# Kernel optimization log

Measured on AMD Instinct MI355X. Metric: run time of the kernel, lower is better.

Reference implementation:

```python
import jax, jax.numpy as jnp
import numpy as np

N_NODES = 50000
N_EDGES = 800000
IN_F = 128
OUT_F = 64
ORDER = 3


def _spmm(edge_index, edge_attr, x):
    # out[row] += edge_attr[e] * x[col]  (COO sparse @ dense)
    row, col = edge_index[0], edge_index[1]
    msgs = x[col] * edge_attr[:, None]          # [E, F] gather + scale
    return jax.ops.segment_sum(msgs, row, num_segments=N_NODES)  # scatter-add


def setup_inputs() -> dict:
    key = jax.random.key(0)
    k1, k2, k3, k4 = jax.random.split(key, 4)
    x = jax.random.normal(k1, (N_NODES, IN_F), dtype=jnp.float32)
    edge_index = jax.random.randint(k2, (2, N_EDGES), 0, N_NODES, dtype=jnp.int64)
    edge_attr = jax.random.uniform(k3, (N_EDGES,), dtype=jnp.float32)
    W = jax.random.normal(k4, (OUT_F, IN_F), dtype=jnp.float32) * (1.0 / np.sqrt(IN_F))
    b = jnp.zeros((OUT_F,), dtype=jnp.float32)
    return {"x": x, "edge_index": edge_index, "edge_attr": edge_attr, "W": W, "b": b}


def reference(x, edge_index, edge_attr, W, b):
    # output = Linear(x); then `order` rounds of spmm aggregation
    out = jnp.einsum("ni,oi->no", x, W) + b      # [N, OUT_F]
    for _ in range(ORDER):
        out = _spmm(edge_index, edge_attr, out)
    return out
```

## Files before the change

kernel.cpp:

```cpp
#include <hip/hip_runtime.h>

#define IN_F   128
#define OUT_F  64
#define GR     64
#define EPB    4096
#define HB     512

typedef float  f32x4  __attribute__((ext_vector_type(4)));
typedef unsigned int u32x2 __attribute__((ext_vector_type(2)));

__device__ __forceinline__ unsigned short f2bf(float f) {
    unsigned int u = __float_as_uint(f);
    u += 0x7fffu + ((u >> 16) & 1u);
    return (unsigned short)(u >> 16);
}
__device__ __forceinline__ float bf2f(unsigned short h) {
    return __uint_as_float(((unsigned int)h) << 16);
}

template <bool BF16OUT>
__global__ __launch_bounds__(256) void gemm_hist_kernel(
    const float* __restrict__ x, const float* __restrict__ W,
    const float* __restrict__ b, void* __restrict__ outv, int N,
    const int* __restrict__ rowi, int* __restrict__ bcnt, int E,
    int gemm_blocks, int hist_blocks) {

    if ((int)blockIdx.x >= gemm_blocks) {
        __shared__ int hcnt[256];
        int t = threadIdx.x;
        hcnt[t] = 0;
        __syncthreads();
        int hb = blockIdx.x - gemm_blocks;
        for (int e = hb * 256 + t; e < E; e += hist_blocks * 256)
            atomicAdd(&hcnt[rowi[e] >> 8], 1);
        __syncthreads();
        if (hcnt[t] > 0) atomicAdd(&bcnt[t], hcnt[t]);
        return;
    }

    __shared__ float xs[GR][IN_F + 4];
    __shared__ float Wt[IN_F][OUT_F + 4];

    const int t = threadIdx.x;
    const int row0 = blockIdx.x * GR;

    for (int i = t; i < OUT_F * (IN_F / 4); i += 256) {
        int o = i & 63;
        int c = i >> 6;
        float4 v = ((const float4*)W)[o * (IN_F / 4) + c];
        Wt[4 * c + 0][o] = v.x;
        Wt[4 * c + 1][o] = v.y;
        Wt[4 * c + 2][o] = v.z;
        Wt[4 * c + 3][o] = v.w;
    }
    for (int i = t; i < GR * (IN_F / 4); i += 256) {
        int r = i >> 5, c = i & 31;
        int gr = row0 + r;
        float4 v = make_float4(0.f, 0.f, 0.f, 0.f);
        if (gr < N) v = ((const float4*)x)[(size_t)gr * (IN_F / 4) + c];
        *(float4*)&xs[r][4 * c] = v;
    }
    __syncthreads();

    const int f0 = (t & 15) * 4;
    const int r0 = (t >> 4) * 4;
    float acc[4][4] = {};

    #pragma unroll 2
    for (int k = 0; k < IN_F; k += 4) {
        float4 xv[4], wv[4];
        #pragma unroll
        for (int i = 0; i < 4; ++i) xv[i] = *(const float4*)&xs[r0 + i][k];
        #pragma unroll
        for (int j = 0; j < 4; ++j) wv[j] = *(const float4*)&Wt[k + j][f0];
        #pragma unroll
        for (int i = 0; i < 4; ++i) {
            #pragma unroll
            for (int j = 0; j < 4; ++j) {
                float wx = j == 0 ? wv[0].x : (j == 1 ? wv[0].y : (j == 2 ? wv[0].z : wv[0].w));
                float wy = j == 0 ? wv[1].x : (j == 1 ? wv[1].y : (j == 2 ? wv[1].z : wv[1].w));
                float wz = j == 0 ? wv[2].x : (j == 1 ? wv[2].y : (j == 2 ? wv[2].z : wv[2].w));
                float ww = j == 0 ? wv[3].x : (j == 1 ? wv[3].y : (j == 2 ? wv[3].z : wv[3].w));
                acc[i][j] = fmaf(xv[i].x, wx, acc[i][j]);
                acc[i][j] = fmaf(xv[i].y, wy, acc[i][j]);
                acc[i][j] = fmaf(xv[i].z, wz, acc[i][j]);
                acc[i][j] = fmaf(xv[i].w, ww, acc[i][j]);
            }
        }
    }

    float4 bv = *(const float4*)&b[f0];
    #pragma unroll
    for (int i = 0; i < 4; ++i) {
        int gr = row0 + r0 + i;
        if (gr < N) {
            float o0 = acc[i][0] + bv.x, o1 = acc[i][1] + bv.y;
            float o2 = acc[i][2] + bv.z, o3 = acc[i][3] + bv.w;
            if (BF16OUT) {
                ushort4 u = { f2bf(o0), f2bf(o1), f2bf(o2), f2bf(o3) };
                *(ushort4*)((unsigned short*)outv + (size_t)gr * OUT_F + f0) = u;
            } else {
                float4 o4 = make_float4(o0, o1, o2, o3);
                *(float4*)((float*)outv + (size_t)gr * OUT_F + f0) = o4;
            }
        }
    }
}

__global__ __launch_bounds__(256) void bscan_kernel(const int* __restrict__ bcnt,
                                                    int* __restrict__ bbase,
                                                    int* __restrict__ bcursor,
                                                    int* __restrict__ rowptr,
                                                    int nb, int N, int E) {
    int t = threadIdx.x;
    int v = (t < nb) ? bcnt[t] : 0;
    int lane = t & 63, w = t >> 6;
    int sum = v;
    #pragma unroll
    for (int off = 1; off < 64; off <<= 1) {
        int x = __shfl_up(sum, off, 64);
        if (lane >= off) sum += x;
    }
    __shared__ int wsum[4];
    if (lane == 63) wsum[w] = sum;
    __syncthreads();
    int woff = 0;
    for (int i = 0; i < w; ++i) woff += wsum[i];
    int excl = sum + woff - v;
    if (t <= nb) bbase[t] = excl;
    if (t < nb)  bcursor[t] = excl;
    if (t == 0)  rowptr[N] = E;
}

__global__ __launch_bounds__(512) void bin_kernel(
    const int* __restrict__ rowi, const int* __restrict__ coli,
    const float* __restrict__ attr, int* __restrict__ bcursor,
    unsigned long long* __restrict__ tmp, int E) {
    __shared__ int cnt[256];
    __shared__ int cur[256];
    __shared__ int gbase[256];
    int t = threadIdx.x;
    int e0 = blockIdx.x * EPB;
    if (t < 256) { cnt[t] = 0; cur[t] = 0; }
    __syncthreads();
    int myrow[8];
    #pragma unroll
    for (int i = 0; i < 8; ++i) {
        int e = e0 + i * 512 + t;
        myrow[i] = (e < E) ? rowi[e] : -1;
        if (myrow[i] >= 0) atomicAdd(&cnt[myrow[i] >> 8], 1);
    }
    __syncthreads();
    if (t < 256 && cnt[t] > 0) gbase[t] = atomicAdd(&bcursor[t], cnt[t]);
    __syncthreads();
    #pragma unroll
    for (int i = 0; i < 8; ++i) {
        int e = e0 + i * 512 + t;
        if (myrow[i] >= 0) {
            int b = myrow[i] >> 8;
            int rank = atomicAdd(&cur[b], 1);
            unsigned long long rec = ((unsigned long long)(myrow[i] & 255) << 32)
                                   | ((unsigned int)coli[e] << 16)
                                   | (unsigned int)f2bf(attr[e]);
            tmp[(size_t)gbase[b] + rank] = rec;
        }
    }
}

__global__ __launch_bounds__(512) void bsort_kernel(
    const unsigned long long* __restrict__ tmp, const int* __restrict__ bbase,
    unsigned int* __restrict__ scv, int* __restrict__ rowptr, int N) {
    __shared__ int cnt[256];
    __shared__ int cur[256];
    __shared__ int wsum[4];
    int t = threadIdx.x, b = blockIdx.x;
    int seg = bbase[b], segend = bbase[b + 1];
    if (t < 256) cnt[t] = 0;
    __syncthreads();
    for (int i = seg + t; i < segend; i += 512)
        atomicAdd(&cnt[(int)(tmp[i] >> 32)], 1);
    __syncthreads();
    if (t < 256) {
        int v = cnt[t];
        int lane = t & 63, w = t >> 6;
        int sum = v;
        #pragma unroll
        for (int off = 1; off < 64; off <<= 1) {
            int x = __shfl_up(sum, off, 64);
            if (lane >= off) sum += x;
        }
        if (lane == 63) wsum[w] = sum;
        __syncthreads();
        int woff = 0;
        for (int i = 0; i < w; ++i) woff += wsum[i];
        int excl = sum + woff - v;
        int gidx = b * 256 + t;
        if (gidx <= N) rowptr[gidx] = seg + excl;
        cur[t] = excl;
    } else {
        __syncthreads();
    }
    __syncthreads();
    for (int i = seg + t; i < segend; i += 512) {
        unsigned long long rec = tmp[i];
        int rl = (int)(rec >> 32);
        int pos = atomicAdd(&cur[rl], 1);
        scv[(size_t)seg + pos] = (unsigned int)rec;
    }
}

#define FMA4(w, p)                                              \
    a0 = fmaf((w), __uint_as_float((p).x << 16), a0);           \
    a1 = fmaf((w), __uint_as_float((p).x & 0xffff0000u), a1);   \
    a2 = fmaf((w), __uint_as_float((p).y << 16), a2);           \
    a3 = fmaf((w), __uint_as_float((p).y & 0xffff0000u), a3)

template <bool BF16OUT>
__global__ __launch_bounds__(256) void spmm_csr_kernel(
    const int* __restrict__ rowptr, const unsigned int* __restrict__ scv,
    const unsigned short* __restrict__ in, void* __restrict__ outv, int N) {
    int wid = (blockIdx.x * 256 + threadIdx.x) >> 6;
    int lane = threadIdx.x & 63;
    if (wid >= N) return;
    wid = __builtin_amdgcn_readfirstlane(wid);
    const unsigned int g = lane >> 4;
    const unsigned int s = lane & 15;
    int beg = rowptr[wid], end = rowptr[wid + 1];
    float a0 = 0.f, a1 = 0.f, a2 = 0.f, a3 = 0.f;

    int e = beg;
    for (; e + 16 <= end; e += 16) {
        unsigned int v0 = scv[e + g];
        unsigned int v1 = scv[e + 4 + g];
        unsigned int v2 = scv[e + 8 + g];
        unsigned int v3 = scv[e + 12 + g];
        u32x2 p0 = *(const u32x2*)(in + ((v0 >> 16) << 6) + (s << 2));
        u32x2 p1 = *(const u32x2*)(in + ((v1 >> 16) << 6) + (s << 2));
        u32x2 p2 = *(const u32x2*)(in + ((v2 >> 16) << 6) + (s << 2));
        u32x2 p3 = *(const u32x2*)(in + ((v3 >> 16) << 6) + (s << 2));
        float w0 = __uint_as_float(v0 << 16);
        float w1 = __uint_as_float(v1 << 16);
        float w2 = __uint_as_float(v2 << 16);
        float w3 = __uint_as_float(v3 << 16);
        FMA4(w0, p0);
        FMA4(w1, p1);
        FMA4(w2, p2);
        FMA4(w3, p3);
    }
    if (e + 8 <= end) {
        unsigned int v0 = scv[e + g];
        unsigned int v1 = scv[e + 4 + g];
        u32x2 p0 = *(const u32x2*)(in + ((v0 >> 16) << 6) + (s << 2));
        u32x2 p1 = *(const u32x2*)(in + ((v1 >> 16) << 6) + (s << 2));
        float w0 = __uint_as_float(v0 << 16);
        float w1 = __uint_as_float(v1 << 16);
        FMA4(w0, p0);
        FMA4(w1, p1);
        e += 8;
    }
    for (; e < end; e += 4) {
        unsigned int v = (e + (int)g < end) ? scv[e + g] : 0u;
        u32x2 p = *(const u32x2*)(in + ((v >> 16) << 6) + (s << 2));
        float w = __uint_as_float(v << 16);
        FMA4(w, p);
    }

    a0 += __shfl_xor(a0, 16); a0 += __shfl_xor(a0, 32);
    a1 += __shfl_xor(a1, 16); a1 += __shfl_xor(a1, 32);
    a2 += __shfl_xor(a2, 16); a2 += __shfl_xor(a2, 32);
    a3 += __shfl_xor(a3, 16); a3 += __shfl_xor(a3, 32);

    if (g == 0) {
        size_t o = (size_t)wid * OUT_F + (s << 2);
        if (BF16OUT) {
            unsigned long long u =  (unsigned long long)f2bf(a0)
                                 | ((unsigned long long)f2bf(a1) << 16)
                                 | ((unsigned long long)f2bf(a2) << 32)
                                 | ((unsigned long long)f2bf(a3) << 48);
            *(unsigned long long*)((unsigned short*)outv + o) = u;
        } else {
            f32x4 o4 = { a0, a1, a2, a3 };
            *(f32x4*)((float*)outv + o) = o4;
        }
    }
}

__global__ __launch_bounds__(256) void spmm_atomic_kernel(
    const int* __restrict__ rowi, const int* __restrict__ coli,
    const float* __restrict__ attr, const float* __restrict__ in,
    float* __restrict__ out, int E) {
    int tid = blockIdx.x * 256 + threadIdx.x;
    int e = tid >> 6;
    int lane = tid & 63;
    if (e >= E) return;
    int r = rowi[e];
    int c = coli[e];
    float w = attr[e];
    float v = in[(size_t)c * OUT_F + lane];
    atomicAdd(&out[(size_t)r * OUT_F + lane], w * v);
}

extern "C" void kernel_launch(void* const* d_in, const int* in_sizes, int n_in,
                              void* d_out, int out_size, void* d_ws, size_t ws_size,
                              hipStream_t stream) {
    const float* x    = (const float*)d_in[0];
    const int*   ei   = (const int*)d_in[1];
    const float* attr = (const float*)d_in[2];
    const float* W    = (const float*)d_in[3];
    const float* b    = (const float*)d_in[4];
    float* out = (float*)d_out;

    const int N = in_sizes[0] / IN_F;
    const int E = in_sizes[2];
    const int* rowi = ei;
    const int* coli = ei + E;

    const size_t obytes_f  = (size_t)N * OUT_F * sizeof(float);
    const size_t obytes_bf = (size_t)N * OUT_F * sizeof(unsigned short);
    const int nb = (N + 255) / 256;

    char* wp = (char*)d_ws;
    size_t off = 0;
    auto alloc = [&](size_t bytes) { char* p = wp + off; off += (bytes + 255) & ~(size_t)255; return p; };
    unsigned short* bufA = (unsigned short*)alloc(obytes_bf);
    unsigned short* bufB = (unsigned short*)alloc((size_t)E * 8);
    unsigned long long* tmp = (unsigned long long*)bufB;
    int* rowptr  = (int*)alloc((size_t)(N + 1) * 4);
    int* bcnt    = (int*)alloc(260 * 4);
    int* bbase   = (int*)alloc(260 * 4);
    int* bcursor = (int*)alloc(260 * 4);
    unsigned int* scv = (unsigned int*)alloc((size_t)E * 4);
    const bool csr_ok = (off <= ws_size) && (N <= 65280) && ((size_t)E * 8 >= obytes_bf);

    const int gemm_blocks = (N + GR - 1) / GR;
    const int sb = (N * 64 + 255) / 256;

    if (csr_ok) {
        hipMemsetAsync(bcnt, 0, 260 * 4, stream);
        gemm_hist_kernel<true><<<gemm_blocks + HB, 256, 0, stream>>>(
            x, W, b, bufA, N, rowi, bcnt, E, gemm_blocks, HB);

        bscan_kernel<<<1, 256, 0, stream>>>(bcnt, bbase, bcursor, rowptr, nb, N, E);
        bin_kernel<<<(E + EPB - 1) / EPB, 512, 0, stream>>>(rowi, coli, attr, bcursor, tmp, E);
        bsort_kernel<<<nb, 512, 0, stream>>>(tmp, bbase, scv, rowptr, N);

        spmm_csr_kernel<true ><<<sb, 256, 0, stream>>>(rowptr, scv, bufA, bufB, N);
        spmm_csr_kernel<true ><<<sb, 256, 0, stream>>>(rowptr, scv, bufB, bufA, N);
        spmm_csr_kernel<false><<<sb, 256, 0, stream>>>(rowptr, scv, bufA, out, N);
    } else {
        float* ws0 = (float*)d_ws;
        gemm_hist_kernel<false><<<gemm_blocks, 256, 0, stream>>>(
            x, W, b, ws0, N, rowi, (int*)d_ws, 0, gemm_blocks, 0);
        const int spmm_blocks = (E * 64 + 255) / 256;
        hipMemsetAsync(out, 0, obytes_f, stream);
        spmm_atomic_kernel<<<spmm_blocks, 256, 0, stream>>>(rowi, coli, attr, ws0, out, E);
        hipMemsetAsync(ws0, 0, obytes_f, stream);
        spmm_atomic_kernel<<<spmm_blocks, 256, 0, stream>>>(rowi, coli, attr, out, ws0, E);
        hipMemsetAsync(out, 0, obytes_f, stream);
        spmm_atomic_kernel<<<spmm_blocks, 256, 0, stream>>>(rowi, coli, attr, ws0, out, E);
    }
}
```

Measured before the change: 191.3 us.

## Split feature dimension into two 32-wide halves for cache-resident SpMM passes

The GEMM output is stored in a feature-split layout of two contiguous halves of 32 bf16 features each, and each SpMM round runs as two launches, one per half. Each half's gathered working set (about 3.2 MB) is half the size of the full matrix and is more likely to stay in L2/MALL during random column gathers. The cost is twice the launches, a second pass over rowptr/scv, an extra shuffle-reduction stage, and 64B gather segments per edge instead of 128B.

```diff
diff --git a/kernel.cpp b/kernel.cpp
--- a/kernel.cpp
+++ b/kernel.cpp
@@ -97,8 +97,13 @@
             float o0 = acc[i][0] + bv.x, o1 = acc[i][1] + bv.y;
             float o2 = acc[i][2] + bv.z, o3 = acc[i][3] + bv.w;
             if (BF16OUT) {
-                ushort4 u = { f2bf(o0), f2bf(o1), f2bf(o2), f2bf(o3) };
-                *(ushort4*)((unsigned short*)outv + (size_t)gr * OUT_F + f0) = u;
+                int hh = f0 >> 5, fo = f0 & 31;
+                unsigned long long u =  (unsigned long long)f2bf(o0)
+                                     | ((unsigned long long)f2bf(o1) << 16)
+                                     | ((unsigned long long)f2bf(o2) << 32)
+                                     | ((unsigned long long)f2bf(o3) << 48);
+                *(unsigned long long*)((unsigned short*)outv
+                    + (size_t)hh * N * 32 + (size_t)gr * 32 + fo) = u;
             } else {
                 float4 o4 = make_float4(o0, o1, o2, o3);
                 *(float4*)((float*)outv + (size_t)gr * OUT_F + f0) = o4;
@@ -216,71 +221,53 @@
     a3 = fmaf((w), __uint_as_float((p).y & 0xffff0000u), a3)
 
 template <bool BF16OUT>
-__global__ __launch_bounds__(256) void spmm_csr_kernel(
+__global__ __launch_bounds__(256) void spmm_half_kernel(
     const int* __restrict__ rowptr, const unsigned int* __restrict__ scv,
-    const unsigned short* __restrict__ in, void* __restrict__ outv, int N) {
+    const unsigned short* __restrict__ inh,
+    void* __restrict__ outv,
+    int N, int h) {
     int wid = (blockIdx.x * 256 + threadIdx.x) >> 6;
     int lane = threadIdx.x & 63;
     if (wid >= N) return;
     wid = __builtin_amdgcn_readfirstlane(wid);
-    const unsigned int g = lane >> 4;
-    const unsigned int s = lane & 15;
+    const unsigned int g = lane >> 3;
+    const unsigned int s = lane & 7;
     int beg = rowptr[wid], end = rowptr[wid + 1];
     float a0 = 0.f, a1 = 0.f, a2 = 0.f, a3 = 0.f;
 
     int e = beg;
     for (; e + 16 <= end; e += 16) {
         unsigned int v0 = scv[e + g];
-        unsigned int v1 = scv[e + 4 + g];
-        unsigned int v2 = scv[e + 8 + g];
-        unsigned int v3 = scv[e + 12 + g];
-        u32x2 p0 = *(const u32x2*)(in + ((v0 >> 16) << 6) + (s << 2));
-        u32x2 p1 = *(const u32x2*)(in + ((v1 >> 16) << 6) + (s << 2));
-        u32x2 p2 = *(const u32x2*)(in + ((v2 >> 16) << 6) + (s << 2));
-        u32x2 p3 = *(const u32x2*)(in + ((v3 >> 16) << 6) + (s << 2));
-        float w0 = __uint_as_float(v0 << 16);
-        float w1 = __uint_as_float(v1 << 16);
-        float w2 = __uint_as_float(v2 << 16);
-        float w3 = __uint_as_float(v3 << 16);
-        FMA4(w0, p0);
-        FMA4(w1, p1);
-        FMA4(w2, p2);
-        FMA4(w3, p3);
-    }
-    if (e + 8 <= end) {
-        unsigned int v0 = scv[e + g];
-        unsigned int v1 = scv[e + 4 + g];
-        u32x2 p0 = *(const u32x2*)(in + ((v0 >> 16) << 6) + (s << 2));
-        u32x2 p1 = *(const u32x2*)(in + ((v1 >> 16) << 6) + (s << 2));
+        unsigned int v1 = scv[e + 8 + g];
+        u32x2 p0 = *(const u32x2*)(inh + ((v0 >> 16) << 5) + (s << 2));
+        u32x2 p1 = *(const u32x2*)(inh + ((v1 >> 16) << 5) + (s << 2));
         float w0 = __uint_as_float(v0 << 16);
         float w1 = __uint_as_float(v1 << 16);
         FMA4(w0, p0);
         FMA4(w1, p1);
-        e += 8;
-    }
-    for (; e < end; e += 4) {
+    }
+    for (; e < end; e += 8) {
         unsigned int v = (e + (int)g < end) ? scv[e + g] : 0u;
-        u32x2 p = *(const u32x2*)(in + ((v >> 16) << 6) + (s << 2));
+        u32x2 p = *(const u32x2*)(inh + ((v >> 16) << 5) + (s << 2));
         float w = __uint_as_float(v << 16);
         FMA4(w, p);
     }
 
-    a0 += __shfl_xor(a0, 16); a0 += __shfl_xor(a0, 32);
-    a1 += __shfl_xor(a1, 16); a1 += __shfl_xor(a1, 32);
-    a2 += __shfl_xor(a2, 16); a2 += __shfl_xor(a2, 32);
-    a3 += __shfl_xor(a3, 16); a3 += __shfl_xor(a3, 32);
+    a0 += __shfl_xor(a0, 8); a0 += __shfl_xor(a0, 16); a0 += __shfl_xor(a0, 32);
+    a1 += __shfl_xor(a1, 8); a1 += __shfl_xor(a1, 16); a1 += __shfl_xor(a1, 32);
+    a2 += __shfl_xor(a2, 8); a2 += __shfl_xor(a2, 16); a2 += __shfl_xor(a2, 32);
+    a3 += __shfl_xor(a3, 8); a3 += __shfl_xor(a3, 16); a3 += __shfl_xor(a3, 32);
 
     if (g == 0) {
-        size_t o = (size_t)wid * OUT_F + (s << 2);
         if (BF16OUT) {
             unsigned long long u =  (unsigned long long)f2bf(a0)
                                  | ((unsigned long long)f2bf(a1) << 16)
                                  | ((unsigned long long)f2bf(a2) << 32)
                                  | ((unsigned long long)f2bf(a3) << 48);
-            *(unsigned long long*)((unsigned short*)outv + o) = u;
+            *(unsigned long long*)((unsigned short*)outv + (size_t)wid * 32 + (s << 2)) = u;
         } else {
             f32x4 o4 = { a0, a1, a2, a3 };
-            *(f32x4*)((float*)outv + o) = o4;
+            *(f32x4*)((float*)outv + (size_t)wid * OUT_F + h * 32 + (s << 2)) = o4;
         }
     }
 }
@@ -334,6 +321,7 @@
 
     const int gemm_blocks = (N + GR - 1) / GR;
     const int sb = (N * 64 + 255) / 256;
+    const size_t HS = (size_t)N * 32;
 
     if (csr_ok) {
         hipMemsetAsync(bcnt, 0, 260 * 4, stream);
@@ -344,9 +332,12 @@
         bin_kernel<<<(E + EPB - 1) / EPB, 512, 0, stream>>>(rowi, coli, attr, bcursor, tmp, E);
         bsort_kernel<<<nb, 512, 0, stream>>>(tmp, bbase, scv, rowptr, N);
 
-        spmm_csr_kernel<true ><<<sb, 256, 0, stream>>>(rowptr, scv, bufA, bufB, N);
-        spmm_csr_kernel<true ><<<sb, 256, 0, stream>>>(rowptr, scv, bufB, bufA, N);
-        spmm_csr_kernel<false><<<sb, 256, 0, stream>>>(rowptr, scv, bufA, out, N);
+        spmm_half_kernel<true ><<<sb, 256, 0, stream>>>(rowptr, scv, bufA,      bufB,      N, 0);
+        spmm_half_kernel<true ><<<sb, 256, 0, stream>>>(rowptr, scv, bufA + HS, bufB + HS, N, 1);
+        spmm_half_kernel<true ><<<sb, 256, 0, stream>>>(rowptr, scv, bufB,      bufA,      N, 0);
+        spmm_half_kernel<true ><<<sb, 256, 0, stream>>>(rowptr, scv, bufB + HS, bufA + HS, N, 1);
+        spmm_half_kernel<false><<<sb, 256, 0, stream>>>(rowptr, scv, bufA,      out,       N, 0);
+        spmm_half_kernel<false><<<sb, 256, 0, stream>>>(rowptr, scv, bufA + HS, out,       N, 1);
     } else {
         float* ws0 = (float*)d_ws;
         gemm_hist_kernel<false><<<gemm_blocks, 256, 0, stream>>>(
```

Result: slower. 229.2 us (+19.8%).

## Use persistent row-looping SpMM waves and per-block histogram partials

Applied to the files above, without the earlier changes.

The CSR SpMM kernel now launches a fixed grid of 2048 blocks, and each wave processes a contiguous range of rows in a loop instead of handling one row per wave. This is meant to cut wave launch and scheduling overhead for the 50k rows. Separately, the histogram blocks are cut from 512 to 64, and each writes its per-block bucket counts to a partials array. The scan kernel sums these partials, which removes the memset and the global atomics. The costs are a serial 64-iteration loop per scan thread and possible load imbalance, since each wave now gets a fixed row range regardless of edge count.

```diff
diff --git a/kernel.cpp b/kernel.cpp
--- a/kernel.cpp
+++ b/kernel.cpp
@@ -4,7 +4,8 @@
 #define OUT_F  64
 #define GR     64
 #define EPB    4096
-#define HB     512
+#define HB     64
+#define SB     2048
 
 typedef float  f32x4  __attribute__((ext_vector_type(4)));
 typedef unsigned int u32x2 __attribute__((ext_vector_type(2)));
@@ -22,7 +23,7 @@
 __global__ __launch_bounds__(256) void gemm_hist_kernel(
     const float* __restrict__ x, const float* __restrict__ W,
     const float* __restrict__ b, void* __restrict__ outv, int N,
-    const int* __restrict__ rowi, int* __restrict__ bcnt, int E,
+    const int* __restrict__ rowi, int* __restrict__ bparts, int E,
     int gemm_blocks, int hist_blocks) {
 
     if ((int)blockIdx.x >= gemm_blocks) {
@@ -34,7 +35,7 @@
         for (int e = hb * 256 + t; e < E; e += hist_blocks * 256)
             atomicAdd(&hcnt[rowi[e] >> 8], 1);
         __syncthreads();
-        if (hcnt[t] > 0) atomicAdd(&bcnt[t], hcnt[t]);
+        bparts[hb * 256 + t] = hcnt[t];
         return;
     }
 
@@ -107,13 +108,15 @@
     }
 }
 
-__global__ __launch_bounds__(256) void bscan_kernel(const int* __restrict__ bcnt,
+__global__ __launch_bounds__(256) void bscan_kernel(const int* __restrict__ bparts,
                                                     int* __restrict__ bbase,
                                                     int* __restrict__ bcursor,
                                                     int* __restrict__ rowptr,
-                                                    int nb, int N, int E) {
+                                                    int nb, int N, int E, int hist_blocks) {
     int t = threadIdx.x;
-    int v = (t < nb) ? bcnt[t] : 0;
+    int v = 0;
+    if (t < nb)
+        for (int hb = 0; hb < hist_blocks; ++hb) v += bparts[hb * 256 + t];
     int lane = t & 63, w = t >> 6;
     int sum = v;
     #pragma unroll
@@ -218,69 +221,76 @@
 template <bool BF16OUT>
 __global__ __launch_bounds__(256) void spmm_csr_kernel(
     const int* __restrict__ rowptr, const unsigned int* __restrict__ scv,
-    const unsigned short* __restrict__ in, void* __restrict__ outv, int N) {
-    int wid = (blockIdx.x * 256 + threadIdx.x) >> 6;
+    const unsigned short* __restrict__ in, void* __restrict__ outv,
+    int N, int nwaves) {
+    int gw = (blockIdx.x * 256 + threadIdx.x) >> 6;
     int lane = threadIdx.x & 63;
-    if (wid >= N) return;
-    wid = __builtin_amdgcn_readfirstlane(wid);
+    int rpw = (N + nwaves - 1) / nwaves;
+    int r0 = gw * rpw;
+    int r1 = r0 + rpw;
+    if (r1 > N) r1 = N;
     const unsigned int g = lane >> 4;
     const unsigned int s = lane & 15;
-    int beg = rowptr[wid], end = rowptr[wid + 1];
-    float a0 = 0.f, a1 = 0.f, a2 = 0.f, a3 = 0.f;
-
-    int e = beg;
-    for (; e + 16 <= end; e += 16) {
-        unsigned int v0 = scv[e + g];
-        unsigned int v1 = scv[e + 4 + g];
-        unsigned int v2 = scv[e + 8 + g];
-        unsigned int v3 = scv[e + 12 + g];
-        u32x2 p0 = *(const u32x2*)(in + ((v0 >> 16) << 6) + (s << 2));
-        u32x2 p1 = *(const u32x2*)(in + ((v1 >> 16) << 6) + (s << 2));
-        u32x2 p2 = *(const u32x2*)(in + ((v2 >> 16) << 6) + (s << 2));
-        u32x2 p3 = *(const u32x2*)(in + ((v3 >> 16) << 6) + (s << 2));
-        float w0 = __uint_as_float(v0 << 16);
-        float w1 = __uint_as_float(v1 << 16);
-        float w2 = __uint_as_float(v2 << 16);
-        float w3 = __uint_as_float(v3 << 16);
-        FMA4(w0, p0);
-        FMA4(w1, p1);
-        FMA4(w2, p2);
-        FMA4(w3, p3);
-    }
-    if (e + 8 <= end) {
-        unsigned int v0 = scv[e + g];
-        unsigned int v1 = scv[e + 4 + g];
-        u32x2 p0 = *(const u32x2*)(in + ((v0 >> 16) << 6) + (s << 2));
-        u32x2 p1 = *(const u32x2*)(in + ((v1 >> 16) << 6) + (s << 2));
-        float w0 = __uint_as_float(v0 << 16);
-        float w1 = __uint_as_float(v1 << 16);
-        FMA4(w0, p0);
-        FMA4(w1, p1);
-        e += 8;
-    }
-    for (; e < end; e += 4) {
-        unsigned int v = (e + (int)g < end) ? scv[e + g] : 0u;
-        u32x2 p = *(const u32x2*)(in + ((v >> 16) << 6) + (s << 2));
-        float w = __uint_as_float(v << 16);
-        FMA4(w, p);
-    }
-
-    a0 += __shfl_xor(a0, 16); a0 += __shfl_xor(a0, 32);
-    a1 += __shfl_xor(a1, 16); a1 += __shfl_xor(a1, 32);
-    a2 += __shfl_xor(a2, 16); a2 += __shfl_xor(a2, 32);
-    a3 += __shfl_xor(a3, 16); a3 += __shfl_xor(a3, 32);
-
-    if (g == 0) {
-        size_t o = (size_t)wid * OUT_F + (s << 2);
-        if (BF16OUT) {
-            unsigned long long u =  (unsigned long long)f2bf(a0)
-                                 | ((unsigned long long)f2bf(a1) << 16)
-                                 | ((unsigned long long)f2bf(a2) << 32)
-                                 | ((unsigned long long)f2bf(a3) << 48);
-            *(unsigned long long*)((unsigned short*)outv + o) = u;
-        } else {
-            f32x4 o4 = { a0, a1, a2, a3 };
-            *(f32x4*)((float*)outv + o) = o4;
+
+    for (int wr = r0; wr < r1; ++wr) {
+        int wid = __builtin_amdgcn_readfirstlane(wr);
+        int beg = rowptr[wid], end = rowptr[wid + 1];
+        float a0 = 0.f, a1 = 0.f, a2 = 0.f, a3 = 0.f;
+
+        int e = beg;
+        for (; e + 16 <= end; e += 16) {
+            unsigned int v0 = scv[e + g];
+            unsigned int v1 = scv[e + 4 + g];
+            unsigned int v2 = scv[e + 8 + g];
+            unsigned int v3 = scv[e + 12 + g];
+            u32x2 p0 = *(const u32x2*)(in + ((v0 >> 16) << 6) + (s << 2));
+            u32x2 p1 = *(const u32x2*)(in + ((v1 >> 16) << 6) + (s << 2));
+            u32x2 p2 = *(const u32x2*)(in + ((v2 >> 16) << 6) + (s << 2));
+            u32x2 p3 = *(const u32x2*)(in + ((v3 >> 16) << 6) + (s << 2));
+            float w0 = __uint_as_float(v0 << 16);
+            float w1 = __uint_as_float(v1 << 16);
+            float w2 = __uint_as_float(v2 << 16);
+            float w3 = __uint_as_float(v3 << 16);
+            FMA4(w0, p0);
+            FMA4(w1, p1);
+            FMA4(w2, p2);
+            FMA4(w3, p3);
+        }
+        if (e + 8 <= end) {
+            unsigned int v0 = scv[e + g];
+            unsigned int v1 = scv[e + 4 + g];
+            u32x2 p0 = *(const u32x2*)(in + ((v0 >> 16) << 6) + (s << 2));
+            u32x2 p1 = *(const u32x2*)(in + ((v1 >> 16) << 6) + (s << 2));
+            float w0 = __uint_as_float(v0 << 16);
+            float w1 = __uint_as_float(v1 << 16);
+            FMA4(w0, p0);
+            FMA4(w1, p1);
+            e += 8;
+        }
+        for (; e < end; e += 4) {
+            unsigned int v = (e + (int)g < end) ? scv[e + g] : 0u;
+            u32x2 p = *(const u32x2*)(in + ((v >> 16) << 6) + (s << 2));
+            float w = __uint_as_float(v << 16);
+            FMA4(w, p);
+        }
+
+        a0 += __shfl_xor(a0, 16); a0 += __shfl_xor(a0, 32);
+        a1 += __shfl_xor(a1, 16); a1 += __shfl_xor(a1, 32);
+        a2 += __shfl_xor(a2, 16); a2 += __shfl_xor(a2, 32);
+        a3 += __shfl_xor(a3, 16); a3 += __shfl_xor(a3, 32);
+
+        if (g == 0) {
+            size_t o = (size_t)wid * OUT_F + (s << 2);
+            if (BF16OUT) {
+                unsigned long long u =  (unsigned long long)f2bf(a0)
+                                     | ((unsigned long long)f2bf(a1) << 16)
+                                     | ((unsigned long long)f2bf(a2) << 32)
+                                     | ((unsigned long long)f2bf(a3) << 48);
+                *(unsigned long long*)((unsigned short*)outv + o) = u;
+            } else {
+                f32x4 o4 = { a0, a1, a2, a3 };
+                *(f32x4*)((float*)outv + o) = o4;
+            }
         }
     }
 }
@@ -326,27 +336,26 @@
     unsigned short* bufB = (unsigned short*)alloc((size_t)E * 8);
     unsigned long long* tmp = (unsigned long long*)bufB;
     int* rowptr  = (int*)alloc((size_t)(N + 1) * 4);
-    int* bcnt    = (int*)alloc(260 * 4);
+    int* bparts  = (int*)alloc((size_t)HB * 256 * 4);
     int* bbase   = (int*)alloc(260 * 4);
     int* bcursor = (int*)alloc(260 * 4);
     unsigned int* scv = (unsigned int*)alloc((size_t)E * 4);
     const bool csr_ok = (off <= ws_size) && (N <= 65280) && ((size_t)E * 8 >= obytes_bf);
 
     const int gemm_blocks = (N + GR - 1) / GR;
-    const int sb = (N * 64 + 255) / 256;
+    const int nwaves = SB * 4;
 
     if (csr_ok) {
-        hipMemsetAsync(bcnt, 0, 260 * 4, stream);
         gemm_hist_kernel<true><<<gemm_blocks + HB, 256, 0, stream>>>(
-            x, W, b, bufA, N, rowi, bcnt, E, gemm_blocks, HB);
-
-        bscan_kernel<<<1, 256, 0, stream>>>(bcnt, bbase, bcursor, rowptr, nb, N, E);
+            x, W, b, bufA, N, rowi, bparts, E, gemm_blocks, HB);
+
+        bscan_kernel<<<1, 256, 0, stream>>>(bparts, bbase, bcursor, rowptr, nb, N, E, HB);
         bin_kernel<<<(E + EPB - 1) / EPB, 512, 0, stream>>>(rowi, coli, attr, bcursor, tmp, E);
         bsort_kernel<<<nb, 512, 0, stream>>>(tmp, bbase, scv, rowptr, N);
 
-        spmm_csr_kernel<true ><<<sb, 256, 0, stream>>>(rowptr, scv, bufA, bufB, N);
-        spmm_csr_kernel<true ><<<sb, 256, 0, stream>>>(rowptr, scv, bufB, bufA, N);
-        spmm_csr_kernel<false><<<sb, 256, 0, stream>>>(rowptr, scv, bufA, out, N);
+        spmm_csr_kernel<true ><<<SB, 256, 0, stream>>>(rowptr, scv, bufA, bufB, N, nwaves);
+        spmm_csr_kernel<true ><<<SB, 256, 0, stream>>>(rowptr, scv, bufB, bufA, N, nwaves);
+        spmm_csr_kernel<false><<<SB, 256, 0, stream>>>(rowptr, scv, bufA, out, N, nwaves);
     } else {
         float* ws0 = (float*)d_ws;
         gemm_hist_kernel<false><<<gemm_blocks, 256, 0, stream>>>(
```

Result: no change. 189.5 us (-1.0%).
